# Performance work log

Hardware: AMD Instinct MI355X
Metric: run time of the kernel (lower is better)

## Reference

```python
import jax, jax.numpy as jnp
import numpy as np
from math import sqrt

B, L, S, H, E, D = 4, 1024, 1024, 16, 64, 64


def setup_inputs() -> dict:
    key = jax.random.key(0)
    k0, k1, k2, k3 = jax.random.split(key, 4)
    queries = jax.random.normal(k0, (B, L, H, E), dtype=jnp.float32)
    keys = jax.random.normal(k1, (B, S, H, E), dtype=jnp.float32)
    values = jax.random.normal(k2, (B, S, H, D), dtype=jnp.float32)
    # RealFormer residual logits from a "previous layer", shape [B,H,L,S]
    prev_logits = jax.random.normal(k3, (B, H, L, S), dtype=jnp.float32) * 0.1
    # Triangular causal mask: True above the diagonal (positions to mask out)
    attn_mask = jnp.triu(jnp.ones((L, S), dtype=bool), k=1)[None, None]  # [1,1,L,S] broadcasts over B
    attn_mask = jnp.broadcast_to(attn_mask, (B, 1, L, S))
    return {"queries": queries, "keys": keys, "values": values,
            "prev_logits": prev_logits, "attn_mask": attn_mask}


def reference(queries, keys, values, prev_logits, attn_mask):
    # queries [B,L,H,E], keys [B,S,H,E], values [B,S,H,D]
    scale = 1.0 / sqrt(queries.shape[-1])
    scores = jnp.einsum('blhe,bshe->bhls', queries, keys) * scale  # [B,H,L,S]
    # RealFormer residual
    scores = scores + prev_logits
    # causal masking with dtype-min (matches torch.finfo(dtype).min masked_fill)
    neg_inf = jnp.finfo(scores.dtype).min
    scores = jnp.where(attn_mask, neg_inf, scores)
    A = jax.nn.softmax(scores, axis=-1)  # dropout p=0.0 -> identity (eval/reference mode)
    # Faithful to source: einsum 'bhls,bshd->bhls' sums only over d,
    # i.e. V[b,h,l,s] = A[b,h,l,s] * sum_d values[b,s,h,d]
    V = jnp.einsum('bhls,bshd->bhls', A, values)  # [B,H,L,S]
    # return_logits=True, output_attention=False -> (V, None, scores); drop the None
    return V, scores
```

## Files before the change

kernel.cpp:

```cpp
#include <hip/hip_runtime.h>
#include <cfloat>

#define B_ 4
#define L_ 1024
#define S_ 1024
#define H_ 16
#define E_ 64
#define TL 32
#define TS 128
#define NT (S_ / TS)

#define MASK_VAL (-3.3895313892515355e38f)

typedef __attribute__((ext_vector_type(8))) short short8;
typedef __attribute__((ext_vector_type(4))) float f32x4;

__device__ __forceinline__ unsigned short f32_to_bf16(float x) {
    unsigned int u = __float_as_uint(x);
    u += 0x7FFFu + ((u >> 16) & 1u);
    return (unsigned short)(u >> 16);
}

__device__ __forceinline__ short8 pack8v(const f32x4 a, const f32x4 b, float s) {
    short8 r;
    r[0] = (short)f32_to_bf16(a[0] * s); r[1] = (short)f32_to_bf16(a[1] * s);
    r[2] = (short)f32_to_bf16(a[2] * s); r[3] = (short)f32_to_bf16(a[3] * s);
    r[4] = (short)f32_to_bf16(b[0] * s); r[5] = (short)f32_to_bf16(b[1] * s);
    r[6] = (short)f32_to_bf16(b[2] * s); r[7] = (short)f32_to_bf16(b[3] * s);
    return r;
}

__device__ __forceinline__ void nt_store4(float* p, float a, float b, float c, float d) {
    f32x4 v = {a, b, c, d};
    __builtin_nontemporal_store(v, (f32x4*)p);
}
__device__ __forceinline__ f32x4 nt_load4(const float* p) {
    return __builtin_nontemporal_load((const f32x4*)p);
}

__global__ __launch_bounds__(256) void vsum_kernel(const float* __restrict__ values,
                                                   float* __restrict__ vsum_t) {
    int t = threadIdx.x;
    int rg = blockIdx.x * 16 + (t >> 4);
    int c = t & 15;
    float4 v = ((const float4*)(values + (long)rg * 64))[c];
    float p = v.x + v.y + v.z + v.w;
    p += __shfl_xor(p, 1);
    p += __shfl_xor(p, 2);
    p += __shfl_xor(p, 4);
    p += __shfl_xor(p, 8);
    if (c == 0) {
        int b = rg >> 14;
        int s = (rg >> 4) & (S_ - 1);
        int h = rg & (H_ - 1);
        vsum_t[(((b << 4) + h) << 10) + s] = p;
    }
}

template <int USE_WS>
__global__ __launch_bounds__(512) void attn_kernel(
    const float* __restrict__ Qg,
    const float* __restrict__ Kg,
    const float* __restrict__ prev,
    const float* __restrict__ vsum,
    const float* __restrict__ values,
    float* __restrict__ outV,
    float* __restrict__ outS)
{
    __shared__ __align__(16) short Ksh[2][TS * E_];
    __shared__ __align__(16) float Dsh[2][TL * TS];
    __shared__ __align__(16) float Vsl[S_];

    const int tid  = threadIdx.x;
    const int lane = tid & 63;
    const int wave = tid >> 6;
    const int bid  = blockIdx.x;
    const int jj   = bid >> 3;
    const int bh   = ((bid & 7) << 3) | (jj & 7);
    const int lt   = 31 - (jj >> 3);
    const int b    = bh >> 4;
    const int h    = bh & 15;
    const int row0 = lt << 5;

    if (USE_WS) {
        if (tid < 256) {
            float4 v = ((const float4*)(vsum + ((long)bh << 10)))[tid];
            *((float4*)&Vsl[tid << 2]) = v;
        }
    } else {
#pragma unroll
        for (int i = 0; i < 2; ++i) {
            int s = tid + (i << 9);
            const float4* vp = (const float4*)(values + (((long)((b << 10) + s) << 10) + (h << 6)));
            float a = 0.f;
#pragma unroll
            for (int j = 0; j < 16; ++j) { float4 t4 = vp[j]; a += t4.x + t4.y + t4.z + t4.w; }
            Vsl[s] = a;
        }
    }

    const int mcol  = lane & 15;
    const int mg    = lane >> 4;
    const int strip = wave & 1;
    const int qrow  = row0 + (strip << 4) + mcol;
    short8 qf0, qf1;
    {
        const float* qp = Qg + (((long)((b << 10) + qrow) << 10) + (h << 6));
        f32x4 a0 = *(const f32x4*)(qp + (mg << 3));
        f32x4 a1 = *(const f32x4*)(qp + (mg << 3) + 4);
        f32x4 a2 = *(const f32x4*)(qp + 32 + (mg << 3));
        f32x4 a3 = *(const f32x4*)(qp + 32 + (mg << 3) + 4);
        qf0 = pack8v(a0, a1, 1.0f);
        qf1 = pack8v(a2, a3, 1.0f);
    }

    const int cg   = lane & 31;
    const int half = lane >> 5;
    const int r0   = (wave << 2) + (half << 1);
    const int r1   = r0 + 1;
    const int rg0  = row0 + r0;
    const int rg1  = row0 + r1;
    const int maxrow = row0 + TL - 1;
    const int NC   = (maxrow >> 7) + 1;
    const long outbase = (long)bh << 20;

    for (int st = NC; st < NT; ++st) {
        const int colb = st * TS + (cg << 2);
        nt_store4(outS + outbase + (long)rg0 * S_ + colb, MASK_VAL, MASK_VAL, MASK_VAL, MASK_VAL);
        nt_store4(outS + outbase + (long)rg1 * S_ + colb, MASK_VAL, MASK_VAL, MASK_VAL, MASK_VAL);
        nt_store4(outV + outbase + (long)rg0 * S_ + colb, 0.f, 0.f, 0.f, 0.f);
        nt_store4(outV + outbase + (long)rg1 * S_ + colb, 0.f, 0.f, 0.f, 0.f);
    }

    const int sr  = tid >> 2;
    const int qtr = tid & 3;
    f32x4 kv0, kv1, kv2, kv3;
#define KLOAD(STC) do { \
        const f32x4* kp = (const f32x4*)(Kg + (((long)((b << 10) + ((STC) * TS + sr)) << 10) + (h << 6) + (qtr << 4))); \
        kv0 = kp[0]; kv1 = kp[1]; kv2 = kp[2]; kv3 = kp[3]; \
    } while (0)

    float ev0[NT][4], ev1[NT][4];
    f32x4 pv0[NT], pv1[NT];
    float sum0 = 0.f, sum1 = 0.f;

    KLOAD(0);
    pv0[0] = nt_load4(prev + outbase + (long)rg0 * S_ + (cg << 2));
    pv1[0] = nt_load4(prev + outbase + (long)rg1 * S_ + (cg << 2));

#define EPI(c) do { \
        const float* DB = &Dsh[(c) & 1][0]; \
        f32x4 d0 = *(const f32x4*)&DB[(r0 << 7) + ((cg ^ (r0 & 7)) << 2)]; \
        f32x4 d1 = *(const f32x4*)&DB[(r1 << 7) + ((cg ^ (r1 & 7)) << 2)]; \
        const int colb = (c) * TS + (cg << 2); \
        float sA[4], sB[4]; \
        _Pragma("unroll") \
        for (int j = 0; j < 4; ++j) { \
            float t0 = d0[j] + pv0[c][j]; \
            float t1 = d1[j] + pv1[c][j]; \
            sA[j] = (colb + j > rg0) ? MASK_VAL : t0; \
            sB[j] = (colb + j > rg1) ? MASK_VAL : t1; \
            float e0 = __expf(sA[j]); ev0[c][j] = e0; sum0 += e0; \
            float e1 = __expf(sB[j]); ev1[c][j] = e1; sum1 += e1; \
        } \
        nt_store4(outS + outbase + (long)rg0 * S_ + colb, sA[0], sA[1], sA[2], sA[3]); \
        nt_store4(outS + outbase + (long)rg1 * S_ + colb, sB[0], sB[1], sB[2], sB[3]); \
    } while (0)

#pragma unroll
    for (int st = 0; st <= NT; ++st) {
        if (st < NC) {
            {
                short* KB = &Ksh[st & 1][0];
                int base = sr << 6;
                int xr = sr & 7;
                *(short8*)&KB[base + ((((qtr << 1) + 0) ^ xr) << 3)] = pack8v(kv0, kv1, 0.125f);
                *(short8*)&KB[base + ((((qtr << 1) + 1) ^ xr) << 3)] = pack8v(kv2, kv3, 0.125f);
            }
            if (st + 1 < NC) {
                KLOAD(st + 1);
                pv0[st + 1] = nt_load4(prev + outbase + (long)rg0 * S_ + (st + 1) * TS + (cg << 2));
                pv1[st + 1] = nt_load4(prev + outbase + (long)rg1 * S_ + (st + 1) * TS + (cg << 2));
            }
            __syncthreads();
            {
                const short* KB = &Ksh[st & 1][0];
                float* DB = &Dsh[st & 1][0];
#pragma unroll
                for (int i = 0; i < 2; ++i) {
                    const int ss  = ((wave >> 1) << 1) + i;
                    const int lsr = (ss << 4) + mcol;
                    const int xr  = mcol & 7;
                    short8 a0 = *(const short8*)&KB[(lsr << 6) + (((0 + mg) ^ xr) << 3)];
                    short8 a1 = *(const short8*)&KB[(lsr << 6) + (((4 + mg) ^ xr) << 3)];
                    f32x4 acc = {0.f, 0.f, 0.f, 0.f};
                    acc = __builtin_amdgcn_mfma_f32_16x16x32_bf16(a0, qf0, acc, 0, 0, 0);
                    acc = __builtin_amdgcn_mfma_f32_16x16x32_bf16(a1, qf1, acc, 0, 0, 0);
                    const int lrow = (strip << 4) + mcol;
                    const int qd   = (ss << 2) + mg;
                    *(f32x4*)&DB[(lrow << 7) + ((qd ^ (lrow & 7)) << 2)] = acc;
                }
            }
        } else if (st == NC) {
            __syncthreads();
        }
        if (st >= 1 && st - 1 < NC) {
            EPI(st - 1);
        }
    }
#undef EPI
#undef KLOAD

#pragma unroll
    for (int m = 1; m <= 16; m <<= 1) {
        sum0 += __shfl_xor(sum0, m);
        sum1 += __shfl_xor(sum1, m);
    }
    const float inv0 = 1.0f / sum0;
    const float inv1 = 1.0f / sum1;

#pragma unroll
    for (int st = 0; st < NT; ++st) {
        if (st < NC) {
            const int colb = st * TS + (cg << 2);
            f32x4 vv = *(const f32x4*)&Vsl[colb];
            nt_store4(outV + outbase + (long)rg0 * S_ + colb,
                      ev0[st][0] * inv0 * vv[0], ev0[st][1] * inv0 * vv[1],
                      ev0[st][2] * inv0 * vv[2], ev0[st][3] * inv0 * vv[3]);
            nt_store4(outV + outbase + (long)rg1 * S_ + colb,
                      ev1[st][0] * inv1 * vv[0], ev1[st][1] * inv1 * vv[1],
                      ev1[st][2] * inv1 * vv[2], ev1[st][3] * inv1 * vv[3]);
        }
    }
}

extern "C" void kernel_launch(void* const* d_in, const int* in_sizes, int n_in,
                              void* d_out, int out_size, void* d_ws, size_t ws_size,
                              hipStream_t stream) {
    const float* Qg   = (const float*)d_in[0];
    const float* Kg   = (const float*)d_in[1];
    const float* Vg   = (const float*)d_in[2];
    const float* prev = (const float*)d_in[3];

    float* outV = (float*)d_out;
    float* outS = outV + (long)B_ * H_ * L_ * S_;

    const size_t vsum_bytes = (size_t)B_ * H_ * S_ * sizeof(float);
    const int grid = B_ * H_ * (L_ / TL);
    if (ws_size >= vsum_bytes) {
        float* vsum_t = (float*)d_ws;
        vsum_kernel<<<(B_ * S_ * H_) / 16, 256, 0, stream>>>(Vg, vsum_t);
        attn_kernel<1><<<grid, 512, 0, stream>>>(Qg, Kg, prev, vsum_t, Vg, outV, outS);
    } else {
        attn_kernel<0><<<grid, 512, 0, stream>>>(Qg, Kg, prev, nullptr, Vg, outV, outS);
    }
}
```

Baseline: 172.2 us.

## Apply epilogue directly on MFMA accumulators, dropping LDS score staging

The softmax epilogue now runs straight on the MFMA accumulator fragments, so the shared-memory score buffer Dsh and its write/read round trip are gone. Row sums are reduced across the four column-quarter waves through a small shared array. Prev-logit loads move from one-tile-ahead prefetch to the current tile, and launch bounds now request 4 waves per SIMD. In exchange, global stores are no longer laid out for full-row coalescing per wave, and the prev loads are less latency-hidden.

Measured after the change: 215.1 us. 24.9% more time.

```diff
diff --git a/kernel.cpp b/kernel.cpp
--- a/kernel.cpp
+++ b/kernel.cpp
@@ -58,7 +58,7 @@
 }
 
 template <int USE_WS>
-__global__ __launch_bounds__(512) void attn_kernel(
+__global__ __launch_bounds__(512, 4) void attn_kernel(
     const float* __restrict__ Qg,
     const float* __restrict__ Kg,
     const float* __restrict__ prev,
@@ -68,8 +68,8 @@
     float* __restrict__ outS)
 {
     __shared__ __align__(16) short Ksh[2][TS * E_];
-    __shared__ __align__(16) float Dsh[2][TL * TS];
     __shared__ __align__(16) float Vsl[S_];
+    __shared__ float Rs[8][16];
 
     const int tid  = threadIdx.x;
     const int lane = tid & 63;
@@ -102,7 +102,14 @@
     const int mcol  = lane & 15;
     const int mg    = lane >> 4;
     const int strip = wave & 1;
+    const int quar  = wave >> 1;
+    const int cb    = quar << 5;
     const int qrow  = row0 + (strip << 4) + mcol;
+    const long outbase = (long)bh << 20;
+    const float* prow = prev + outbase + ((long)qrow << 10);
+    float* srow = outS + outbase + ((long)qrow << 10);
+    float* vrow = outV + outbase + ((long)qrow << 10);
+
     short8 qf0, qf1;
     {
         const float* qp = Qg + (((long)((b << 10) + qrow) << 10) + (h << 6));
@@ -114,22 +121,15 @@
         qf1 = pack8v(a2, a3, 1.0f);
     }
 
-    const int cg   = lane & 31;
-    const int half = lane >> 5;
-    const int r0   = (wave << 2) + (half << 1);
-    const int r1   = r0 + 1;
-    const int rg0  = row0 + r0;
-    const int rg1  = row0 + r1;
     const int maxrow = row0 + TL - 1;
-    const int NC   = (maxrow >> 7) + 1;
-    const long outbase = (long)bh << 20;
+    const int NC = (maxrow >> 7) + 1;
 
     for (int st = NC; st < NT; ++st) {
-        const int colb = st * TS + (cg << 2);
-        nt_store4(outS + outbase + (long)rg0 * S_ + colb, MASK_VAL, MASK_VAL, MASK_VAL, MASK_VAL);
-        nt_store4(outS + outbase + (long)rg1 * S_ + colb, MASK_VAL, MASK_VAL, MASK_VAL, MASK_VAL);
-        nt_store4(outV + outbase + (long)rg0 * S_ + colb, 0.f, 0.f, 0.f, 0.f);
-        nt_store4(outV + outbase + (long)rg1 * S_ + colb, 0.f, 0.f, 0.f, 0.f);
+        const int c0 = st * TS + cb + (mg << 2);
+        nt_store4(srow + c0,      MASK_VAL, MASK_VAL, MASK_VAL, MASK_VAL);
+        nt_store4(srow + c0 + 16, MASK_VAL, MASK_VAL, MASK_VAL, MASK_VAL);
+        nt_store4(vrow + c0,      0.f, 0.f, 0.f, 0.f);
+        nt_store4(vrow + c0 + 16, 0.f, 0.f, 0.f, 0.f);
     }
 
     const int sr  = tid >> 2;
@@ -140,35 +140,13 @@
         kv0 = kp[0]; kv1 = kp[1]; kv2 = kp[2]; kv3 = kp[3]; \
     } while (0)
 
-    float ev0[NT][4], ev1[NT][4];
-    f32x4 pv0[NT], pv1[NT];
-    float sum0 = 0.f, sum1 = 0.f;
-
     KLOAD(0);
-    pv0[0] = nt_load4(prev + outbase + (long)rg0 * S_ + (cg << 2));
-    pv1[0] = nt_load4(prev + outbase + (long)rg1 * S_ + (cg << 2));
-
-#define EPI(c) do { \
-        const float* DB = &Dsh[(c) & 1][0]; \
-        f32x4 d0 = *(const f32x4*)&DB[(r0 << 7) + ((cg ^ (r0 & 7)) << 2)]; \
-        f32x4 d1 = *(const f32x4*)&DB[(r1 << 7) + ((cg ^ (r1 & 7)) << 2)]; \
-        const int colb = (c) * TS + (cg << 2); \
-        float sA[4], sB[4]; \
-        _Pragma("unroll") \
-        for (int j = 0; j < 4; ++j) { \
-            float t0 = d0[j] + pv0[c][j]; \
-            float t1 = d1[j] + pv1[c][j]; \
-            sA[j] = (colb + j > rg0) ? MASK_VAL : t0; \
-            sB[j] = (colb + j > rg1) ? MASK_VAL : t1; \
-            float e0 = __expf(sA[j]); ev0[c][j] = e0; sum0 += e0; \
-            float e1 = __expf(sB[j]); ev1[c][j] = e1; sum1 += e1; \
-        } \
-        nt_store4(outS + outbase + (long)rg0 * S_ + colb, sA[0], sA[1], sA[2], sA[3]); \
-        nt_store4(outS + outbase + (long)rg1 * S_ + colb, sB[0], sB[1], sB[2], sB[3]); \
-    } while (0)
-
-#pragma unroll
-    for (int st = 0; st <= NT; ++st) {
+
+    float ev[NT][2][4];
+    float psum = 0.f;
+
+#pragma unroll
+    for (int st = 0; st < NT; ++st) {
         if (st < NC) {
             {
                 short* KB = &Ksh[st & 1][0];
@@ -177,59 +155,60 @@
                 *(short8*)&KB[base + ((((qtr << 1) + 0) ^ xr) << 3)] = pack8v(kv0, kv1, 0.125f);
                 *(short8*)&KB[base + ((((qtr << 1) + 1) ^ xr) << 3)] = pack8v(kv2, kv3, 0.125f);
             }
-            if (st + 1 < NC) {
-                KLOAD(st + 1);
-                pv0[st + 1] = nt_load4(prev + outbase + (long)rg0 * S_ + (st + 1) * TS + (cg << 2));
-                pv1[st + 1] = nt_load4(prev + outbase + (long)rg1 * S_ + (st + 1) * TS + (cg << 2));
+            if (st + 1 < NC) KLOAD(st + 1);
+            const int c0 = st * TS + cb + (mg << 2);
+            f32x4 pA = nt_load4(prow + c0);
+            f32x4 pB = nt_load4(prow + c0 + 16);
+
+            __syncthreads();
+
+            const short* KB = &Ksh[st & 1][0];
+#pragma unroll
+            for (int i = 0; i < 2; ++i) {
+                const int ss  = (quar << 1) + i;
+                const int lsr = (ss << 4) + mcol;
+                const int xr  = mcol & 7;
+                short8 a0 = *(const short8*)&KB[(lsr << 6) + (((0 + mg) ^ xr) << 3)];
+                short8 a1 = *(const short8*)&KB[(lsr << 6) + (((4 + mg) ^ xr) << 3)];
+                f32x4 acc = {0.f, 0.f, 0.f, 0.f};
+                acc = __builtin_amdgcn_mfma_f32_16x16x32_bf16(a0, qf0, acc, 0, 0, 0);
+                acc = __builtin_amdgcn_mfma_f32_16x16x32_bf16(a1, qf1, acc, 0, 0, 0);
+                const int ci = c0 + (i << 4);
+                const f32x4 pp = i ? pB : pA;
+                float sc[4];
+#pragma unroll
+                for (int j = 0; j < 4; ++j) {
+                    float t = acc[j] + pp[j];
+                    sc[j] = (ci + j > qrow) ? MASK_VAL : t;
+                    float e = __expf(sc[j]);
+                    ev[st][i][j] = e;
+                    psum += e;
+                }
+                nt_store4(srow + ci, sc[0], sc[1], sc[2], sc[3]);
             }
-            __syncthreads();
-            {
-                const short* KB = &Ksh[st & 1][0];
-                float* DB = &Dsh[st & 1][0];
-#pragma unroll
-                for (int i = 0; i < 2; ++i) {
-                    const int ss  = ((wave >> 1) << 1) + i;
-                    const int lsr = (ss << 4) + mcol;
-                    const int xr  = mcol & 7;
-                    short8 a0 = *(const short8*)&KB[(lsr << 6) + (((0 + mg) ^ xr) << 3)];
-                    short8 a1 = *(const short8*)&KB[(lsr << 6) + (((4 + mg) ^ xr) << 3)];
-                    f32x4 acc = {0.f, 0.f, 0.f, 0.f};
-                    acc = __builtin_amdgcn_mfma_f32_16x16x32_bf16(a0, qf0, acc, 0, 0, 0);
-                    acc = __builtin_amdgcn_mfma_f32_16x16x32_bf16(a1, qf1, acc, 0, 0, 0);
-                    const int lrow = (strip << 4) + mcol;
-                    const int qd   = (ss << 2) + mg;
-                    *(f32x4*)&DB[(lrow << 7) + ((qd ^ (lrow & 7)) << 2)] = acc;
-                }
-            }
-        } else if (st == NC) {
-            __syncthreads();
-        }
-        if (st >= 1 && st - 1 < NC) {
-            EPI(st - 1);
-        }
-    }
-#undef EPI
+        }
+    }
 #undef KLOAD
 
-#pragma unroll
-    for (int m = 1; m <= 16; m <<= 1) {
-        sum0 += __shfl_xor(sum0, m);
-        sum1 += __shfl_xor(sum1, m);
-    }
-    const float inv0 = 1.0f / sum0;
-    const float inv1 = 1.0f / sum1;
+    psum += __shfl_xor(psum, 16);
+    psum += __shfl_xor(psum, 32);
+    if (mg == 0) Rs[wave][mcol] = psum;
+    __syncthreads();
+    const float inv = 1.0f / (Rs[strip][mcol] + Rs[2 + strip][mcol] +
+                              Rs[4 + strip][mcol] + Rs[6 + strip][mcol]);
 
 #pragma unroll
     for (int st = 0; st < NT; ++st) {
         if (st < NC) {
-            const int colb = st * TS + (cg << 2);
-            f32x4 vv = *(const f32x4*)&Vsl[colb];
-            nt_store4(outV + outbase + (long)rg0 * S_ + colb,
-                      ev0[st][0] * inv0 * vv[0], ev0[st][1] * inv0 * vv[1],
-                      ev0[st][2] * inv0 * vv[2], ev0[st][3] * inv0 * vv[3]);
-            nt_store4(outV + outbase + (long)rg1 * S_ + colb,
-                      ev1[st][0] * inv1 * vv[0], ev1[st][1] * inv1 * vv[1],
-                      ev1[st][2] * inv1 * vv[2], ev1[st][3] * inv1 * vv[3]);
+            const int c0 = st * TS + cb + (mg << 2);
+#pragma unroll
+            for (int i = 0; i < 2; ++i) {
+                const int ci = c0 + (i << 4);
+                f32x4 vv = *(const f32x4*)&Vsl[ci];
+                nt_store4(vrow + ci,
+                          ev[st][i][0] * inv * vv[0], ev[st][i][1] * inv * vv[1],
+                          ev[st][i][2] * inv * vv[2], ev[st][i][3] * inv * vv[3]);
+            }
         }
     }
 }
```
